# Kernel optimization log

Measured on AMD Instinct MI355X. Metric: run time of the kernel, lower is better.

Reference implementation:

```python
import jax, jax.numpy as jnp
import numpy as np
import math

C = 512
EPS = 1e-5


def _ln(x, g, b):
    m = jnp.mean(x, axis=-1, keepdims=True)
    v = jnp.var(x, axis=-1, keepdims=True)
    return (x - m) * jax.lax.rsqrt(v + EPS) * g + b


def _attn(x, w_qkv, w_out):
    # x: (..., L, C); attention over axis -2 (axial)
    qkv = jnp.einsum('...lc,dc->...ld', x, w_qkv)          # (..., L, 3C)
    qkv = qkv.reshape(*qkv.shape[:-1], C, 3)               # interleaved split as in torch reshape(*shape,3)
    q, k, v = qkv[..., 0], qkv[..., 1], qkv[..., 2]
    scale = 1.0 / math.sqrt(C)
    logits = jnp.einsum('...qc,...kc->...qk', q, k) * scale
    p = jax.nn.softmax(logits, axis=-1)
    ctx = jnp.einsum('...qk,...kc->...qc', p, v)
    return jnp.einsum('...lc,dc->...ld', ctx, w_out)


def setup_inputs() -> dict:
    key = jax.random.key(0)
    ks = jax.random.split(key, 16)
    s = 0.02
    inp = {
        'x': jax.random.normal(ks[0], (8, C, 48, 192), jnp.float32),
        'w_qkv1': jax.random.normal(ks[1], (3 * C, C), jnp.float32) * s,
        'w_out1': jax.random.normal(ks[2], (C, C), jnp.float32) * s,
        'w_qkv2': jax.random.normal(ks[3], (3 * C, C), jnp.float32) * s,
        'w_out2': jax.random.normal(ks[4], (C, C), jnp.float32) * s,
        'g1': jnp.ones((C,), jnp.float32), 'b1': jnp.zeros((C,), jnp.float32),
        'g2': jnp.ones((C,), jnp.float32), 'b2': jnp.zeros((C,), jnp.float32),
        'g3': jnp.ones((C,), jnp.float32), 'b3': jnp.zeros((C,), jnp.float32),
        'w_fc1': jax.random.normal(ks[5], (4 * C, C), jnp.float32) * s,
        'b_fc1': jnp.zeros((4 * C,), jnp.float32),
        'w_fc2': jax.random.normal(ks[6], (C, 4 * C), jnp.float32) * s,
        'b_fc2': jnp.zeros((C,), jnp.float32),
    }
    return inp


def reference(x, w_qkv1, w_out1, w_qkv2, w_out2, g1, b1, g2, b2, g3, b3,
              w_fc1, b_fc1, w_fc2, b_fc2):
    # x: (B, C, H, W) -> (B, W, H, C)
    x = jnp.transpose(x, (0, 3, 2, 1))
    x = x + _attn(_ln(x, g1, b1), w_qkv1, w_out1)          # attention along H
    # (B, W, H, C) -> (B, H, W, C)
    x = jnp.transpose(x, (0, 2, 1, 3))
    x = x + _attn(_ln(x, g2, b2), w_qkv2, w_out2)          # attention along W
    h = _ln(x, g3, b3)
    h = jax.nn.relu(jnp.einsum('bhwc,dc->bhwd', h, w_fc1) + b_fc1)
    x = x + jnp.einsum('bhwd,cd->bhwc', h, w_fc2) + b_fc2
    # (B, H, W, C) -> (B, C, H, W)
    return jnp.transpose(x, (0, 3, 1, 2))
```

## Files before the change

### kernel.cpp

```cpp
#include <hip/hip_runtime.h>

typedef unsigned short u16;
typedef __attribute__((ext_vector_type(8))) short short8;
typedef __attribute__((ext_vector_type(8))) __bf16 bf16x8;
typedef __attribute__((ext_vector_type(4))) float f32x4;

#define DEV __device__ __forceinline__

DEV u16 f2bf(float f){ unsigned u = __float_as_uint(f); return (u16)((u + 0x7fffu + ((u>>16)&1u)) >> 16); }
DEV float bf2f(u16 h){ return __uint_as_float(((unsigned)h)<<16); }

DEV f32x4 mfma_bf16(short8 a, short8 b, f32x4 c){
  return __builtin_amdgcn_mfma_f32_16x16x32_bf16(
      __builtin_bit_cast(bf16x8, a), __builtin_bit_cast(bf16x8, b), c, 0, 0, 0);
}

DEV void gl2lds16(const u16* g, u16* s){
  __builtin_amdgcn_global_load_lds(
      (__attribute__((address_space(1))) void*)(g),
      (__attribute__((address_space(3))) void*)(s), 16, 0, 0);
}

#define BB 8
#define HH 48
#define WW 192
#define CC 512
#define NTOK (BB*HH*WW)

__global__ void k_permqkv(const float* __restrict__ w, u16* __restrict__ o){
  int i = blockIdx.x*256 + threadIdx.x;
  int n = i >> 9, kk = i & 511;
  int src = 3*(n & 511) + (n >> 9);
  o[i] = f2bf(w[src*512 + kk]);
}
__global__ void k_conv(const float* __restrict__ w, u16* __restrict__ o, int nelem){
  int i = blockIdx.x*256 + threadIdx.x;
  if (i < nelem) o[i] = f2bf(w[i]);
}

__global__ void k_tin(const float* __restrict__ x, float* __restrict__ xr){
  __shared__ float T[32][33];
  int bh = blockIdx.x / 96, rem = blockIdx.x % 96;
  int c0 = (rem/6)*32, w0 = (rem%6)*32;
  int b = bh / HH, h = bh % HH;
  const float* xp = x + ((size_t)b*CC*HH + h)*WW;
  #pragma unroll
  for (int p=0;p<4;p++){
    int idx = p*256 + threadIdx.x;
    int cc = idx >> 5, ww = idx & 31;
    T[cc][ww] = xp[(size_t)(c0+cc)*(HH*WW) + w0 + ww];
  }
  __syncthreads();
  float* xo = xr + (size_t)bh*WW*CC;
  #pragma unroll
  for (int p=0;p<4;p++){
    int idx = p*256 + threadIdx.x;
    int ww = idx >> 5, cc = idx & 31;
    xo[(size_t)(w0+ww)*CC + c0 + cc] = T[cc][ww];
  }
}

__global__ void k_tout(const float* __restrict__ xr, float* __restrict__ out){
  __shared__ float T[32][33];
  int bh = blockIdx.x / 96, rem = blockIdx.x % 96;
  int c0 = (rem/6)*32, w0 = (rem%6)*32;
  int b = bh / HH, h = bh % HH;
  const float* xi = xr + (size_t)bh*WW*CC;
  #pragma unroll
  for (int p=0;p<4;p++){
    int idx = p*256 + threadIdx.x;
    int ww = idx >> 5, cc = idx & 31;
    T[ww][cc] = xi[(size_t)(w0+ww)*CC + c0 + cc];
  }
  __syncthreads();
  float* op = out + ((size_t)b*CC*HH + h)*WW;
  #pragma unroll
  for (int p=0;p<4;p++){
    int idx = p*256 + threadIdx.x;
    int cc = idx >> 5, ww = idx & 31;
    op[(size_t)(c0+cc)*(HH*WW) + w0 + ww] = T[ww][cc];
  }
}

__global__ void k_ln(const float* __restrict__ xr, const float* __restrict__ g,
                     const float* __restrict__ bb, u16* __restrict__ y){
  int t = blockIdx.x*4 + (threadIdx.x>>6);
  int lane = threadIdx.x & 63;
  const float* row = xr + (size_t)t*CC + lane*8;
  float v[8];
  *(f32x4*)(v)   = *(const f32x4*)(row);
  *(f32x4*)(v+4) = *(const f32x4*)(row+4);
  float s=0.f, s2=0.f;
  #pragma unroll
  for (int j=0;j<8;j++){ s += v[j]; s2 += v[j]*v[j]; }
  #pragma unroll
  for (int o=32;o;o>>=1){ s += __shfl_xor(s,o); s2 += __shfl_xor(s2,o); }
  float mean = s*(1.f/CC);
  float var  = s2*(1.f/CC) - mean*mean;
  float rs = rsqrtf(var + 1e-5f);
  const float* gp = g + lane*8; const float* bp = bb + lane*8;
  short8 o8;
  #pragma unroll
  for (int j=0;j<8;j++) o8[j] = (short)f2bf((v[j]-mean)*rs*gp[j] + bp[j]);
  *(short8*)(y + (size_t)t*CC + lane*8) = o8;
}

__global__ __launch_bounds__(256)
void k_gemm(const u16* __restrict__ A, int lda,
            const u16* __restrict__ Bw, int ldb,
            void* __restrict__ Out, int ldo,
            const float* __restrict__ bias,
            int K, int nbn, int epi){
  __shared__ __align__(16) u16 As[128*32];
  __shared__ __align__(16) u16 Bs[128*32];
  int mb = blockIdx.x / nbn, nb = blockIdx.x % nbn;
  int tid = threadIdx.x, lane = tid & 63, wv = tid >> 6;
  size_t m0 = (size_t)mb*128, n0 = (size_t)nb*128;
  const u16* gA = A  + (m0 + wv*32 + (lane>>2))*(size_t)lda + (lane&3)*8;
  const u16* gB = Bw + (n0 + wv*32 + (lane>>2))*(size_t)ldb + (lane&3)*8;
  u16* sA = As + wv*1024;
  u16* sB = Bs + wv*1024;
  int m = lane & 15, quad = lane >> 4;
  int wm = (wv>>1)*64, wn = (wv&1)*64;
  f32x4 acc[4][4];
  #pragma unroll
  for (int i=0;i<4;i++)
    #pragma unroll
    for (int j=0;j<4;j++) acc[i][j] = (f32x4){0.f,0.f,0.f,0.f};
  const u16* aB = As + (wm + m)*32 + quad*8;
  const u16* bB = Bs + (wn + m)*32 + quad*8;
  for (int k0 = 0; k0 < K; k0 += 32){
    gl2lds16(gA,                  sA);
    gl2lds16(gA + 16*(size_t)lda, sA + 512);
    gl2lds16(gB,                  sB);
    gl2lds16(gB + 16*(size_t)ldb, sB + 512);
    gA += 32; gB += 32;
    __syncthreads();
    short8 af[4], bf[4];
    #pragma unroll
    for (int i=0;i<4;i++) af[i] = *(const short8*)(aB + i*16*32);
    #pragma unroll
    for (int j=0;j<4;j++) bf[j] = *(const short8*)(bB + j*16*32);
    #pragma unroll
    for (int i=0;i<4;i++)
      #pragma unroll
      for (int j=0;j<4;j++)
        acc[i][j] = mfma_bf16(af[i], bf[j], acc[i][j]);
    __syncthreads();
  }
  if (epi == 2){
    float* O = (float*)Out + (m0 + wm + quad*4)*(size_t)ldo + n0 + wn + m;
    #pragma unroll
    for (int j=0;j<4;j++){
      float bv = bias ? bias[n0 + wn + j*16 + m] : 0.f;
      #pragma unroll
      for (int i=0;i<4;i++)
        #pragma unroll
        for (int r=0;r<4;r++)
          O[(size_t)(i*16+r)*ldo + j*16] += acc[i][j][r] + bv;
    }
  } else {
    u16* O = (u16*)Out + (m0 + wm + quad*4)*(size_t)ldo + n0 + wn + m;
    #pragma unroll
    for (int j=0;j<4;j++){
      float bv = bias ? bias[n0 + wn + j*16 + m] : 0.f;
      #pragma unroll
      for (int i=0;i<4;i++)
        #pragma unroll
        for (int r=0;r<4;r++){
          float v = acc[i][j][r] + bv;
          if (epi == 1) v = fmaxf(v, 0.f);
          O[(size_t)(i*16+r)*ldo + j*16] = f2bf(v);
        }
    }
  }
}

__global__ void k_qk(const u16* __restrict__ q, const u16* __restrict__ kp, int ldq,
                     float* __restrict__ S, int L, int nt,
                     int SD, int OUTs, int INN, int LST, float scale){
  int blk = blockIdx.x;
  int s = blk / (nt*nt), tl = blk % (nt*nt);
  int ti = tl / nt, tj = tl % nt;
  int lane = threadIdx.x, m = lane & 15, quad = lane >> 4;
  size_t tokbase = (size_t)(s/SD)*OUTs + (size_t)(s%SD)*INN;
  const u16* qr = q  + (tokbase + (size_t)(ti*16+m)*LST)*ldq + quad*8;
  const u16* kr = kp + (tokbase + (size_t)(tj*16+m)*LST)*ldq + quad*8;
  f32x4 acc = (f32x4){0.f,0.f,0.f,0.f};
  #pragma unroll
  for (int kk=0; kk<CC; kk+=32)
    acc = mfma_bf16(*(const short8*)(qr+kk), *(const short8*)(kr+kk), acc);
  float* Sp = S + (size_t)s*L*L + (size_t)(ti*16 + quad*4)*L + tj*16 + m;
  #pragma unroll
  for (int r=0;r<4;r++) Sp[(size_t)r*L] = acc[r]*scale;
}

__global__ void k_softmax(const float* __restrict__ S, u16* __restrict__ P, int L, int Lp){
  int row = blockIdx.x*4 + (threadIdx.x>>6);
  int lane = threadIdx.x & 63;
  const float* sr = S + (size_t)row*L;
  float v0 = (lane      < L) ? sr[lane]      : -3.0e38f;
  float v1 = (lane+64   < L) ? sr[lane+64]   : -3.0e38f;
  float v2 = (lane+128  < L) ? sr[lane+128]  : -3.0e38f;
  float mx = fmaxf(v0, fmaxf(v1, v2));
  #pragma unroll
  for (int o=32;o;o>>=1) mx = fmaxf(mx, __shfl_xor(mx, o));
  float e0 = (lane      < L) ? __expf(v0-mx) : 0.f;
  float e1 = (lane+64   < L) ? __expf(v1-mx) : 0.f;
  float e2 = (lane+128  < L) ? __expf(v2-mx) : 0.f;
  float sm = e0+e1+e2;
  #pragma unroll
  for (int o=32;o;o>>=1) sm += __shfl_xor(sm, o);
  float inv = 1.f/sm;
  u16* pr = P + (size_t)row*Lp;
  if (lane      < Lp) pr[lane]      = f2bf(e0*inv);
  if (lane+64   < Lp) pr[lane+64]   = f2bf(e1*inv);
  if (lane+128  < Lp) pr[lane+128]  = f2bf(e2*inv);
}

__global__ void k_vt(const u16* __restrict__ v, int ldv, u16* __restrict__ vt,
                     int L, int Lp, int SD, int OUTs, int INN, int LST){
  __shared__ float T[32*193];
  int s = blockIdx.x >> 4;
  int c0 = (blockIdx.x & 15)*32;
  size_t tokbase = (size_t)(s/SD)*OUTs + (size_t)(s%SD)*INN;
  int pad = Lp + 1;
  for (int idx = threadIdx.x; idx < L*32; idx += 256){
    int l = idx >> 5, cc = idx & 31;
    T[cc*pad + l] = bf2f(v[(tokbase + (size_t)l*LST)*ldv + c0 + cc]);
  }
  __syncthreads();
  u16* vo = vt + ((size_t)s*CC + c0)*Lp;
  for (int idx = threadIdx.x; idx < 32*Lp; idx += 256){
    int cc = idx / Lp, l = idx - cc*Lp;
    vo[idx] = (l < L) ? f2bf(T[cc*pad + l]) : (u16)0;
  }
}

template<int L, int Lp, int NTQ, int NCJ>
__global__ __launch_bounds__(256)
void k_pv2(const u16* __restrict__ P, const u16* __restrict__ vt, u16* __restrict__ ctx,
           int SD, int OUTs, int INN, int LST){
  constexpr int G   = 32 / NCJ;
  constexpr int LPP = Lp + 8;
  constexpr int CW  = NCJ * 16;
  constexpr int CJW = NCJ / 4;
  constexpr int NKS = Lp / 32;
  constexpr int SHW = (L*LPP > L*CW) ? L*LPP : L*CW;
  __shared__ __align__(16) u16 SH[SHW];

  int sq = blockIdx.x / G, g = blockIdx.x % G;
  int tid = threadIdx.x, lane = tid & 63, wv = tid >> 6;
  int m = lane & 15, quad = lane >> 4;

  const u16* Pg = P + (size_t)sq * L * Lp;
  constexpr int PU = L * Lp / 8;
  for (int u = tid; u < PU; u += 256){
    int r = u / (Lp/8), c = u % (Lp/8);
    *(short8*)(SH + r*LPP + c*8) = *(const short8*)(Pg + (size_t)r*Lp + c*8);
  }
  __syncthreads();

  short8 bf[CJW][NKS];
  #pragma unroll
  for (int lc = 0; lc < CJW; lc++){
    const u16* vr = vt + ((size_t)sq*CC + (size_t)((g*NCJ + (wv*CJW + lc))*16 + m))*Lp + quad*8;
    #pragma unroll
    for (int ks = 0; ks < NKS; ks++) bf[lc][ks] = *(const short8*)(vr + ks*32);
  }

  f32x4 acc[CJW][NTQ];
  #pragma unroll
  for (int lc = 0; lc < CJW; lc++)
    #pragma unroll
    for (int qt = 0; qt < NTQ; qt++) acc[lc][qt] = (f32x4){0.f,0.f,0.f,0.f};

  #pragma unroll
  for (int qt = 0; qt < NTQ; qt++){
    short8 a[NKS];
    #pragma unroll
    for (int ks = 0; ks < NKS; ks++)
      a[ks] = *(const short8*)(SH + (qt*16 + m)*LPP + quad*8 + ks*32);
    #pragma unroll
    for (int lc = 0; lc < CJW; lc++)
      #pragma unroll
      for (int ks = 0; ks < NKS; ks++)
        acc[lc][qt] = mfma_bf16(a[ks], bf[lc][ks], acc[lc][qt]);
  }
  __syncthreads();

  #pragma unroll
  for (int qt = 0; qt < NTQ; qt++)
    #pragma unroll
    for (int lc = 0; lc < CJW; lc++)
      #pragma unroll
      for (int r = 0; r < 4; r++)
        SH[(qt*16 + quad*4 + r)*CW + (wv*CJW + lc)*16 + m] = f2bf(acc[lc][qt][r]);
  __syncthreads();

  size_t tokbase = (size_t)(sq/SD)*OUTs + (size_t)(sq%SD)*INN;
  constexpr int CU8 = CW / 8;
  constexpr int TU = L * CU8;
  for (int u = tid; u < TU; u += 256){
    int l = u / CU8, c = u % CU8;
    *(short8*)(ctx + (tokbase + (size_t)l*LST)*CC + g*CW + c*8) =
        *(const short8*)(SH + l*CW + c*8);
  }
}

extern "C" void kernel_launch(void* const* d_in, const int* in_sizes, int n_in,
                              void* d_out, int out_size, void* d_ws, size_t ws_size,
                              hipStream_t stream){
  const float* x      = (const float*)d_in[0];
  const float* wqkv1  = (const float*)d_in[1];
  const float* wout1  = (const float*)d_in[2];
  const float* wqkv2  = (const float*)d_in[3];
  const float* wout2  = (const float*)d_in[4];
  const float* g1 = (const float*)d_in[5];  const float* b1 = (const float*)d_in[6];
  const float* g2 = (const float*)d_in[7];  const float* b2 = (const float*)d_in[8];
  const float* g3 = (const float*)d_in[9];  const float* b3 = (const float*)d_in[10];
  const float* wfc1 = (const float*)d_in[11]; const float* bfc1 = (const float*)d_in[12];
  const float* wfc2 = (const float*)d_in[13]; const float* bfc2 = (const float*)d_in[14];

  char* ws = (char*)d_ws;
  size_t off = 0;
  auto alloc = [&](size_t bytes)->char*{
    char* p = ws + off; off += (bytes + 255) & ~(size_t)255; return p;
  };
  float* xres = (float*)alloc((size_t)NTOK*CC*4);
  u16*   y    = (u16*)  alloc((size_t)NTOK*CC*2);
  u16*   qkv  = (u16*)  alloc((size_t)NTOK*1536*2);
  u16* wqkv1p = (u16*)alloc((size_t)1536*512*2);
  u16* wqkv2p = (u16*)alloc((size_t)1536*512*2);
  u16* wout1p = (u16*)alloc((size_t)512*512*2);
  u16* wout2p = (u16*)alloc((size_t)512*512*2);
  u16* wfc1p  = (u16*)alloc((size_t)2048*512*2);
  u16* wfc2p  = (u16*)alloc((size_t)512*2048*2);
  u16*   hv   = qkv;

  u16*   P    = (u16*)d_out;
  u16*   vt   = (u16*)((char*)d_out + 28311552);
  float* S    = (float*)((char*)d_out + 28311552);
  (void)ws_size; (void)in_sizes; (void)n_in; (void)out_size;

  const float scale = 0.044194173824159216f;

  k_permqkv<<<3072, 256, 0, stream>>>(wqkv1, wqkv1p);
  k_permqkv<<<3072, 256, 0, stream>>>(wqkv2, wqkv2p);
  k_conv<<<1024, 256, 0, stream>>>(wout1, wout1p, 512*512);
  k_conv<<<1024, 256, 0, stream>>>(wout2, wout2p, 512*512);
  k_conv<<<4096, 256, 0, stream>>>(wfc1, wfc1p, 2048*512);
  k_conv<<<4096, 256, 0, stream>>>(wfc2, wfc2p, 512*2048);

  k_tin<<<BB*HH*96, 256, 0, stream>>>(x, xres);

  k_ln<<<NTOK/4, 256, 0, stream>>>(xres, g1, b1, y);
  k_gemm<<<576*12, 256, 0, stream>>>(y, 512, wqkv1p, 512, qkv, 1536, nullptr, 512, 12, 0);
  k_qk<<<1536*9, 64, 0, stream>>>(qkv, qkv+512, 1536, S, 48, 3, 192, 9216, 1, 192, scale);
  k_softmax<<<NTOK/4, 256, 0, stream>>>(S, P, 48, 64);
  k_vt<<<1536*16, 256, 0, stream>>>(qkv+1024, 1536, vt, 48, 64, 192, 9216, 1, 192);
  k_pv2<48,64,3,16><<<1536*2, 256, 0, stream>>>(P, vt, y, 192, 9216, 1, 192);
  k_gemm<<<576*4, 256, 0, stream>>>(y, 512, wout1p, 512, xres, 512, nullptr, 512, 4, 2);

  k_ln<<<NTOK/4, 256, 0, stream>>>(xres, g2, b2, y);
  k_gemm<<<576*12, 256, 0, stream>>>(y, 512, wqkv2p, 512, qkv, 1536, nullptr, 512, 12, 0);
  k_qk<<<384*144, 64, 0, stream>>>(qkv, qkv+512, 1536, S, 192, 12, 48, 9216, 192, 1, scale);
  k_softmax<<<NTOK/4, 256, 0, stream>>>(S, P, 192, 192);
  k_vt<<<384*16, 256, 0, stream>>>(qkv+1024, 1536, vt, 192, 192, 48, 9216, 192, 1);
  k_pv2<192,192,12,8><<<384*4, 256, 0, stream>>>(P, vt, y, 48, 9216, 192, 1);
  k_gemm<<<576*4, 256, 0, stream>>>(y, 512, wout2p, 512, xres, 512, nullptr, 512, 4, 2);

  k_ln<<<NTOK/4, 256, 0, stream>>>(xres, g3, b3, y);
  k_gemm<<<576*8, 256, 0, stream>>>(y, 512, wfc1p, 512, hv, 1024, bfc1, 512, 8, 1);
  k_gemm<<<576*4, 256, 0, stream>>>(hv, 1024, wfc2p, 2048, xres, 512, bfc2, 1024, 4, 2);
  k_gemm<<<576*8, 256, 0, stream>>>(y, 512, wfc1p + 1024*512, 512, hv, 1024, bfc1 + 1024, 512, 8, 1);
  k_gemm<<<576*4, 256, 0, stream>>>(hv, 1024, wfc2p + 1024, 2048, xres, 512, nullptr, 1024, 4, 2);

  k_tout<<<BB*HH*96, 256, 0, stream>>>(xres, (float*)d_out);
}
```

Measured before the change: 2.462 ms.

## Double GEMM K-tile with XOR-swizzled LDS and split MLP by token halves

The GEMM kernel now stages a 64-wide K slice per iteration instead of 32, using an XOR swizzle on the LDS column chunks to avoid bank conflicts, which halves the number of barriers per K loop. The MLP is restructured from two hidden-dimension halves (each doing fc1 then fc2 with K=1024 accumulation) into two token halves, each computing the full 2048-wide hidden and a single fc2 with K=2048. This cuts repeated read-modify-write of the fp32 residual and reuses the LN output once per token. It doubles LDS use per block, which may reduce occupancy.

```diff
diff --git a/kernel.cpp b/kernel.cpp
--- a/kernel.cpp
+++ b/kernel.cpp
@@ -111,41 +111,60 @@
             void* __restrict__ Out, int ldo,
             const float* __restrict__ bias,
             int K, int nbn, int epi){
-  __shared__ __align__(16) u16 As[128*32];
-  __shared__ __align__(16) u16 Bs[128*32];
+  __shared__ __align__(16) u16 As[128*64];
+  __shared__ __align__(16) u16 Bs[128*64];
   int mb = blockIdx.x / nbn, nb = blockIdx.x % nbn;
   int tid = threadIdx.x, lane = tid & 63, wv = tid >> 6;
   size_t m0 = (size_t)mb*128, n0 = (size_t)nb*128;
-  const u16* gA = A  + (m0 + wv*32 + (lane>>2))*(size_t)lda + (lane&3)*8;
-  const u16* gB = Bw + (n0 + wv*32 + (lane>>2))*(size_t)ldb + (lane&3)*8;
-  u16* sA = As + wv*1024;
-  u16* sB = Bs + wv*1024;
+  int lr = lane >> 3;
+  int cc0 = (lane & 7) ^ lr;
+  const u16* gA = A  + (m0 + wv*32 + lr)*(size_t)lda + cc0*8;
+  const u16* gB = Bw + (n0 + wv*32 + lr)*(size_t)ldb + cc0*8;
+  u16* sA = As + wv*32*64;
+  u16* sB = Bs + wv*32*64;
   int m = lane & 15, quad = lane >> 4;
   int wm = (wv>>1)*64, wn = (wv&1)*64;
+  int off0 = ((quad    ) ^ (m & 7))*8;
+  int off1 = ((quad + 4) ^ (m & 7))*8;
   f32x4 acc[4][4];
   #pragma unroll
   for (int i=0;i<4;i++)
     #pragma unroll
     for (int j=0;j<4;j++) acc[i][j] = (f32x4){0.f,0.f,0.f,0.f};
-  const u16* aB = As + (wm + m)*32 + quad*8;
-  const u16* bB = Bs + (wn + m)*32 + quad*8;
-  for (int k0 = 0; k0 < K; k0 += 32){
-    gl2lds16(gA,                  sA);
-    gl2lds16(gA + 16*(size_t)lda, sA + 512);
-    gl2lds16(gB,                  sB);
-    gl2lds16(gB + 16*(size_t)ldb, sB + 512);
-    gA += 32; gB += 32;
+  const u16* aB = As + (wm + m)*64;
+  const u16* bB = Bs + (wn + m)*64;
+  for (int k0 = 0; k0 < K; k0 += 64){
+    #pragma unroll
+    for (int t=0;t<4;t++){
+      gl2lds16(gA + (size_t)(t*8)*lda, sA + t*8*64);
+      gl2lds16(gB + (size_t)(t*8)*ldb, sB + t*8*64);
+    }
+    gA += 64; gB += 64;
     __syncthreads();
-    short8 af[4], bf[4];
-    #pragma unroll
-    for (int i=0;i<4;i++) af[i] = *(const short8*)(aB + i*16*32);
-    #pragma unroll
-    for (int j=0;j<4;j++) bf[j] = *(const short8*)(bB + j*16*32);
-    #pragma unroll
-    for (int i=0;i<4;i++)
-      #pragma unroll
-      for (int j=0;j<4;j++)
-        acc[i][j] = mfma_bf16(af[i], bf[j], acc[i][j]);
+    {
+      short8 af[4], bf[4];
+      #pragma unroll
+      for (int i=0;i<4;i++) af[i] = *(const short8*)(aB + i*16*64 + off0);
+      #pragma unroll
+      for (int j=0;j<4;j++) bf[j] = *(const short8*)(bB + j*16*64 + off0);
+      #pragma unroll
+      for (int i=0;i<4;i++)
+        #pragma unroll
+        for (int j=0;j<4;j++)
+          acc[i][j] = mfma_bf16(af[i], bf[j], acc[i][j]);
+    }
+    {
+      short8 af[4], bf[4];
+      #pragma unroll
+      for (int i=0;i<4;i++) af[i] = *(const short8*)(aB + i*16*64 + off1);
+      #pragma unroll
+      for (int j=0;j<4;j++) bf[j] = *(const short8*)(bB + j*16*64 + off1);
+      #pragma unroll
+      for (int i=0;i<4;i++)
+        #pragma unroll
+        for (int j=0;j<4;j++)
+          acc[i][j] = mfma_bf16(af[i], bf[j], acc[i][j]);
+    }
     __syncthreads();
   }
   if (epi == 2){
@@ -261,12 +280,12 @@
   }
   __syncthreads();
 
-  short8 bf[CJW][NKS];
+  short8 bfr[CJW][NKS];
   #pragma unroll
   for (int lc = 0; lc < CJW; lc++){
     const u16* vr = vt + ((size_t)sq*CC + (size_t)((g*NCJ + (wv*CJW + lc))*16 + m))*Lp + quad*8;
     #pragma unroll
-    for (int ks = 0; ks < NKS; ks++) bf[lc][ks] = *(const short8*)(vr + ks*32);
+    for (int ks = 0; ks < NKS; ks++) bfr[lc][ks] = *(const short8*)(vr + ks*32);
   }
 
   f32x4 acc[CJW][NTQ];
@@ -285,7 +304,7 @@
     for (int lc = 0; lc < CJW; lc++)
       #pragma unroll
       for (int ks = 0; ks < NKS; ks++)
-        acc[lc][qt] = mfma_bf16(a[ks], bf[lc][ks], acc[lc][qt]);
+        acc[lc][qt] = mfma_bf16(a[ks], bfr[lc][ks], acc[lc][qt]);
   }
   __syncthreads();
 
@@ -371,10 +390,11 @@
   k_gemm<<<576*4, 256, 0, stream>>>(y, 512, wout2p, 512, xres, 512, nullptr, 512, 4, 2);
 
   k_ln<<<NTOK/4, 256, 0, stream>>>(xres, g3, b3, y);
-  k_gemm<<<576*8, 256, 0, stream>>>(y, 512, wfc1p, 512, hv, 1024, bfc1, 512, 8, 1);
-  k_gemm<<<576*4, 256, 0, stream>>>(hv, 1024, wfc2p, 2048, xres, 512, bfc2, 1024, 4, 2);
-  k_gemm<<<576*8, 256, 0, stream>>>(y, 512, wfc1p + 1024*512, 512, hv, 1024, bfc1 + 1024, 512, 8, 1);
-  k_gemm<<<576*4, 256, 0, stream>>>(hv, 1024, wfc2p + 1024, 2048, xres, 512, nullptr, 1024, 4, 2);
+  for (int half = 0; half < 2; half++){
+    size_t M0 = (size_t)half * 36864;
+    k_gemm<<<288*16, 256, 0, stream>>>(y + M0*512, 512, wfc1p, 512, hv, 2048, bfc1, 512, 16, 1);
+    k_gemm<<<288*4, 256, 0, stream>>>(hv, 2048, wfc2p, 2048, xres + M0*512, 512, bfc2, 2048, 4, 2);
+  }
 
   k_tout<<<BB*HH*96, 256, 0, stream>>>(xres, (float*)d_out);
 }
```

Measured after the change: 2.180 ms. 11.4% less time.
